# Optimization experiments

Measured on AMD Instinct MI355X. Metric: run time of the kernel, lower is better.

The kernel has to match this reference:

```python
import jax, jax.numpy as jnp
import numpy as np

SEQ, BATCH, IN, HID, OUT = 1024, 2048, 32, 12, 1


def setup_inputs() -> dict:
    key = jax.random.key(0)
    ks = jax.random.split(key, 12)
    s = 0.1
    return {
        "X": jax.random.normal(ks[0], (SEQ, BATCH, IN), dtype=jnp.float32),
        # layer 0 (PyTorch gate order: i, f, g, o)
        "Wih0": jax.random.normal(ks[1], (4 * HID, IN), dtype=jnp.float32) * s,
        "Whh0": jax.random.normal(ks[2], (4 * HID, HID), dtype=jnp.float32) * s,
        "bih0": jax.random.normal(ks[3], (4 * HID,), dtype=jnp.float32) * s,
        "bhh0": jax.random.normal(ks[4], (4 * HID,), dtype=jnp.float32) * s,
        # layer 1
        "Wih1": jax.random.normal(ks[5], (4 * HID, HID), dtype=jnp.float32) * s,
        "Whh1": jax.random.normal(ks[6], (4 * HID, HID), dtype=jnp.float32) * s,
        "bih1": jax.random.normal(ks[7], (4 * HID,), dtype=jnp.float32) * s,
        "bhh1": jax.random.normal(ks[8], (4 * HID,), dtype=jnp.float32) * s,
        # final linear head
        "Wfc": jax.random.normal(ks[9], (OUT, HID), dtype=jnp.float32) * s,
        "bfc": jax.random.normal(ks[10], (OUT,), dtype=jnp.float32) * s,
    }


def _lstm_layer(xs, Wih, Whh, bih, bhh):
    # xs: [S, B, D] seq-first, PyTorch nn.LSTM semantics (gate order i,f,g,o)
    B = xs.shape[1]
    H = Whh.shape[1]
    h0 = jnp.zeros((B, H), xs.dtype)
    c0 = jnp.zeros((B, H), xs.dtype)
    b = bih + bhh

    def step(carry, x_t):
        h, c = carry
        z = x_t @ Wih.T + h @ Whh.T + b  # [B, 4H]
        i, f, g, o = jnp.split(z, 4, axis=-1)
        c = jax.nn.sigmoid(f) * c + jax.nn.sigmoid(i) * jnp.tanh(g)
        h = jax.nn.sigmoid(o) * jnp.tanh(c)
        return (h, c), h

    _, hs = jax.lax.scan(step, (h0, c0), xs)
    return hs  # [S, B, H]


def reference(X, Wih0, Whh0, bih0, bhh0, Wih1, Whh1, bih1, bhh1, Wfc, bfc):
    out = _lstm_layer(X, Wih0, Whh0, bih0, bhh0)
    out = _lstm_layer(out, Wih1, Whh1, bih1, bhh1)
    # faithful to original: out[:, -1, :] on seq-first output selects the
    # LAST BATCH element for every timestep -> [S, H]
    last = out[:, -1, :]
    return last @ Wfc.T + bfc  # [S, OUT]
```

## Files before the change

kernel.cpp:

```cpp
#include <hip/hip_runtime.h>

#define SEQ    1024
#define NBATCH 2048
#define INDIM  32
#define HID    12
#define G4     48
#define NB     (SEQ / 4)
#define NBLK   (NB + 4)
#define CHUNK  16
#define NCH    (SEQ / CHUNK)

#define LOG2E 1.4426950408889634f

typedef float f32x2 __attribute__((ext_vector_type(2)));
typedef float f32x4 __attribute__((ext_vector_type(4)));

template<int CTRL>
__device__ __forceinline__ float qbcast(float v) {
    int x = __builtin_amdgcn_update_dpp(
        0, __builtin_bit_cast(int, v), CTRL, 0xF, 0xF, true);
    return __builtin_bit_cast(float, x);
}
__device__ __forceinline__ float lanebcast(float v, int lane) {
    return __builtin_bit_cast(float,
        __builtin_amdgcn_readlane(__builtin_bit_cast(int, v), lane));
}
__device__ __forceinline__ float sig_part(float zs) {
    return __builtin_amdgcn_rcpf(1.0f + __builtin_amdgcn_exp2f(zs));
}

__global__ __launch_bounds__(256) void lstm_pre(
    const float* __restrict__ X,
    const float* __restrict__ Wih0,
    const float* __restrict__ bih0,
    const float* __restrict__ bhh0,
    float* __restrict__ zx)
{
    int idx = blockIdx.x * blockDim.x + threadIdx.x;
    if (idx >= NBLK * 192) return;
    int b   = idx / 192;
    int rem = idx - b * 192;
    int j   = rem >> 2;
    int q   = rem & 3;
    int t   = 4 * b + q;
    if (t >= SEQ) { zx[idx] = 0.0f; return; }
    int g = j & 3, k = j >> 2;
    int r = g * HID + k;
    const float cexpg = (g == 2) ? (-2.0f * LOG2E) : (-LOG2E);
    const float* x = X + (size_t)t * NBATCH * INDIM + (size_t)(NBATCH - 1) * INDIM;
    const float* w = Wih0 + r * INDIM;
    float za = bih0[r] + bhh0[r], zb = 0.0f;
    #pragma unroll
    for (int kk = 0; kk < INDIM; kk += 2) {
        za = fmaf(w[kk],     x[kk],     za);
        zb = fmaf(w[kk + 1], x[kk + 1], zb);
    }
    zx[idx] = (za + zb) * cexpg;
}

__global__ __launch_bounds__(128) void lstm_seq2(
    const f32x4* __restrict__ zx4,
    float* __restrict__ hbuf,
    const float* __restrict__ Whh0,
    const float* __restrict__ Wih1,
    const float* __restrict__ Whh1,
    const float* __restrict__ bih1,
    const float* __restrict__ bhh1)
{
    __shared__ alignas(16) float lds_h0[(SEQ + 4) * HID];

    const int tid  = threadIdx.x;
    const int wave = tid >> 6;
    const int lane = tid & 63;
    const int jj = (lane < G4) ? lane : 0;
    const int g  = jj & 3;
    const int k  = jj >> 2;
    const int r  = g * HID + k;
    const float cexp = (g == 2) ? (-2.0f * LOG2E) : (-LOG2E);
    const float TSA = -4.0f * LOG2E;
    const float TSB =  2.0f * LOG2E;

    f32x4 wh0[3];
    f32x4 zbE[4], zbO[4];
    f32x4 ph0[3];  float cs0 = 0.0f;
    f32x4 wi1[3], wh1[3];
    f32x4 hb0[4][3], hb1[4][3];
    f32x4 ph1[3];  float cs1 = 0.0f;
    float b1s = 0.0f;

    #pragma unroll
    for (int m = 0; m < 3; ++m) { ph0[m] = f32x4{0,0,0,0}; ph1[m] = f32x4{0,0,0,0}; }

    if (wave == 0) {
        if (lane < G4) lds_h0[SEQ * HID + lane] = 0.0f;
        #pragma unroll
        for (int m = 0; m < 3; ++m)
            wh0[m] = *(const f32x4*)(Whh0 + r * HID + 4 * m) * cexp;
        #pragma unroll
        for (int bb = 0; bb < 4; ++bb) zbE[bb] = zx4[bb * G4 + jj];
    } else {
        #pragma unroll
        for (int m = 0; m < 3; ++m) {
            wi1[m] = *(const f32x4*)(Wih1 + r * HID + 4 * m) * cexp;
            wh1[m] = *(const f32x4*)(Whh1 + r * HID + 4 * m) * cexp;
        }
        b1s = (bih1[r] + bhh1[r]) * cexp;
    }
    __syncthreads();

#define STEPA(zs, t) { \
    f32x4 a0 = __builtin_elementwise_fma(wh0[0], ph0[0], f32x4{(zs), 0.f, 0.f, 0.f}); \
    f32x4 a1 = __builtin_elementwise_fma(wh0[1], ph0[1], f32x4{0.f, 0.f, 0.f, 0.f}); \
    f32x4 a2 = __builtin_elementwise_fma(wh0[2], ph0[2], f32x4{0.f, 0.f, 0.f, 0.f}); \
    f32x4 sv = (a0 + a1) + a2; \
    float z  = (sv.x + sv.y) + (sv.z + sv.w); \
    float rr = sig_part(z); \
    float ai = qbcast<0x00>(rr), af = qbcast<0x55>(rr); \
    float ag = qbcast<0xAA>(rr), ao = qbcast<0xFF>(rr); \
    float igs = ai * fmaf(TSA, ag, TSB); \
    cs0 = fmaf(af, cs0, igs); \
    float rt = sig_part(cs0); \
    float h0 = fmaf(ao + ao, rt, -ao); \
    if (lane < G4 && g == 0) lds_h0[(t) * HID + k] = h0; \
    ph0[0] = f32x4{lanebcast(h0, 0),  lanebcast(h0, 4),  lanebcast(h0, 8),  lanebcast(h0, 12)}; \
    ph0[1] = f32x4{lanebcast(h0, 16), lanebcast(h0, 20), lanebcast(h0, 24), lanebcast(h0, 28)}; \
    ph0[2] = f32x4{lanebcast(h0, 32), lanebcast(h0, 36), lanebcast(h0, 40), lanebcast(h0, 44)}; \
}

#define AITER(cur, nxt, ci) { \
    int cb = 4 * ((ci) + 1); \
    nxt[0] = zx4[(cb + 0) * G4 + jj]; \
    nxt[1] = zx4[(cb + 1) * G4 + jj]; \
    nxt[2] = zx4[(cb + 2) * G4 + jj]; \
    nxt[3] = zx4[(cb + 3) * G4 + jj]; \
    int tA = CHUNK * (ci); \
    STEPA(cur[0].x, tA + 0)  STEPA(cur[0].y, tA + 1)  STEPA(cur[0].z, tA + 2)  STEPA(cur[0].w, tA + 3)  \
    STEPA(cur[1].x, tA + 4)  STEPA(cur[1].y, tA + 5)  STEPA(cur[1].z, tA + 6)  STEPA(cur[1].w, tA + 7)  \
    STEPA(cur[2].x, tA + 8)  STEPA(cur[2].y, tA + 9)  STEPA(cur[2].z, tA + 10) STEPA(cur[2].w, tA + 11) \
    STEPA(cur[3].x, tA + 12) STEPA(cur[3].y, tA + 13) STEPA(cur[3].z, tA + 14) STEPA(cur[3].w, tA + 15) \
}

#define LDGRP(trow, dst) { \
    dst[0][0] = *(const f32x4*)&lds_h0[((trow) + 0) * HID + 0]; \
    dst[0][1] = *(const f32x4*)&lds_h0[((trow) + 0) * HID + 4]; \
    dst[0][2] = *(const f32x4*)&lds_h0[((trow) + 0) * HID + 8]; \
    dst[1][0] = *(const f32x4*)&lds_h0[((trow) + 1) * HID + 0]; \
    dst[1][1] = *(const f32x4*)&lds_h0[((trow) + 1) * HID + 4]; \
    dst[1][2] = *(const f32x4*)&lds_h0[((trow) + 1) * HID + 8]; \
    dst[2][0] = *(const f32x4*)&lds_h0[((trow) + 2) * HID + 0]; \
    dst[2][1] = *(const f32x4*)&lds_h0[((trow) + 2) * HID + 4]; \
    dst[2][2] = *(const f32x4*)&lds_h0[((trow) + 2) * HID + 8]; \
    dst[3][0] = *(const f32x4*)&lds_h0[((trow) + 3) * HID + 0]; \
    dst[3][1] = *(const f32x4*)&lds_h0[((trow) + 3) * HID + 4]; \
    dst[3][2] = *(const f32x4*)&lds_h0[((trow) + 3) * HID + 8]; \
}

#define STEPB(cur, qi, t) { \
    f32x4 a0 = __builtin_elementwise_fma(wi1[0], cur[qi][0], f32x4{b1s, 0.f, 0.f, 0.f}); \
    f32x4 a1 = __builtin_elementwise_fma(wi1[1], cur[qi][1], f32x4{0.f, 0.f, 0.f, 0.f}); \
    f32x4 a2 = __builtin_elementwise_fma(wi1[2], cur[qi][2], f32x4{0.f, 0.f, 0.f, 0.f}); \
    a0 = __builtin_elementwise_fma(wh1[0], ph1[0], a0); \
    a1 = __builtin_elementwise_fma(wh1[1], ph1[1], a1); \
    a2 = __builtin_elementwise_fma(wh1[2], ph1[2], a2); \
    f32x4 sv = (a0 + a1) + a2; \
    float z  = (sv.x + sv.y) + (sv.z + sv.w); \
    float rr = sig_part(z); \
    float ai = qbcast<0x00>(rr), af = qbcast<0x55>(rr); \
    float ag = qbcast<0xAA>(rr), ao = qbcast<0xFF>(rr); \
    float igs = ai * fmaf(TSA, ag, TSB); \
    cs1 = fmaf(af, cs1, igs); \
    float rt = sig_part(cs1); \
    float h1 = fmaf(ao + ao, rt, -ao); \
    if (lane < G4 && g == 0) hbuf[(t) * HID + k] = h1; \
    ph1[0] = f32x4{lanebcast(h1, 0),  lanebcast(h1, 4),  lanebcast(h1, 8),  lanebcast(h1, 12)}; \
    ph1[1] = f32x4{lanebcast(h1, 16), lanebcast(h1, 20), lanebcast(h1, 24), lanebcast(h1, 28)}; \
    ph1[2] = f32x4{lanebcast(h1, 32), lanebcast(h1, 36), lanebcast(h1, 40), lanebcast(h1, 44)}; \
}

#define BGRP(cur, nxt, tload, tproc) { \
    LDGRP((tload), nxt) \
    STEPB(cur, 0, (tproc) + 0) STEPB(cur, 1, (tproc) + 1) \
    STEPB(cur, 2, (tproc) + 2) STEPB(cur, 3, (tproc) + 3) \
}

    for (int i = 0; i < NCH + 2; ++i) {
        if (wave == 0) {
            if (i < NCH) {
                if ((i & 1) == 0) { AITER(zbE, zbO, i) }
                else              { AITER(zbO, zbE, i) }
            }
        } else {
            if (i >= 2) {
                int t0 = (i - 2) * CHUNK;
                if (i == 2) { LDGRP(0, hb0) }
                BGRP(hb0, hb1, t0 + 4,  t0)
                BGRP(hb1, hb0, t0 + 8,  t0 + 4)
                BGRP(hb0, hb1, t0 + 12, t0 + 8)
                BGRP(hb1, hb0, t0 + 16, t0 + 12)
            }
        }
        __syncthreads();
    }
#undef STEPA
#undef AITER
#undef LDGRP
#undef STEPB
#undef BGRP
}

__global__ __launch_bounds__(256) void fc_head(
    const float* __restrict__ hbuf,
    const float* __restrict__ Wfc,
    const float* __restrict__ bfc,
    float* __restrict__ out)
{
    int t = blockIdx.x * blockDim.x + threadIdx.x;
    if (t >= SEQ) return;
    float o = bfc[0];
    const float* h = hbuf + t * HID;
    #pragma unroll
    for (int kk = 0; kk < HID; ++kk) o = fmaf(Wfc[kk], h[kk], o);
    out[t] = o;
}

__global__ __launch_bounds__(64) void lstm_seq_fb(
    const float* __restrict__ X,
    const float* __restrict__ Wih0,
    const float* __restrict__ bih0,
    const float* __restrict__ bhh0,
    const float* __restrict__ Whh0,
    const float* __restrict__ Wih1,
    const float* __restrict__ Whh1,
    const float* __restrict__ bih1,
    const float* __restrict__ bhh1,
    const float* __restrict__ Wfc,
    const float* __restrict__ bfc,
    float* __restrict__ out)
{
    const int j  = threadIdx.x;
    const int jj = (j < G4) ? j : 0;
    const int g  = jj & 3;
    const int k  = jj >> 2;
    const int r  = g * HID + k;
    const float cexp = (g == 2) ? (-2.0f * LOG2E) : (-LOG2E);
    const float TSA = -4.0f * LOG2E;
    const float TSB =  2.0f * LOG2E;

    float whh0[HID], wih1[HID], whh1[HID], wih0[INDIM], wfc[HID];
    #pragma unroll
    for (int kk = 0; kk < HID; ++kk) {
        whh0[kk] = Whh0[r * HID + kk] * cexp;
        wih1[kk] = Wih1[r * HID + kk] * cexp;
        whh1[kk] = Whh1[r * HID + kk] * cexp;
        wfc[kk]  = Wfc[kk];
    }
    #pragma unroll
    for (int kk = 0; kk < INDIM; ++kk) wih0[kk] = Wih0[r * INDIM + kk] * cexp;
    const float b0 = (bih0[r] + bhh0[r]) * cexp;
    const float b1 = (bih1[r] + bhh1[r]) * cexp;
    const float bias_fc = bfc[0];

    float h0v[HID], h1v[HID];
    #pragma unroll
    for (int kk = 0; kk < HID; ++kk) { h0v[kk] = 0.0f; h1v[kk] = 0.0f; }
    float cs0 = 0.0f, cs1 = 0.0f;

    for (int t = 0; t < SEQ; ++t) {
        const float* x = X + (size_t)t * NBATCH * INDIM
                           + (size_t)(NBATCH - 1) * INDIM;
        float z0 = b0;
        #pragma unroll
        for (int kk = 0; kk < INDIM; ++kk) z0 = fmaf(wih0[kk], x[kk], z0);
        #pragma unroll
        for (int kk = 0; kk < HID; ++kk) z0 = fmaf(whh0[kk], h0v[kk], z0);
        float rr = sig_part(z0);
        float ai = qbcast<0x00>(rr), af = qbcast<0x55>(rr);
        float ag = qbcast<0xAA>(rr), ao = qbcast<0xFF>(rr);
        cs0 = fmaf(af, cs0, ai * fmaf(TSA, ag, TSB));
        float rt = sig_part(cs0);
        float h0 = fmaf(ao + ao, rt, -ao);
        #pragma unroll
        for (int kk = 0; kk < HID; ++kk) h0v[kk] = lanebcast(h0, 4 * kk);

        float z1 = b1;
        #pragma unroll
        for (int kk = 0; kk < HID; ++kk) {
            z1 = fmaf(wih1[kk], h0v[kk], z1);
            z1 = fmaf(whh1[kk], h1v[kk], z1);
        }
        rr = sig_part(z1);
        ai = qbcast<0x00>(rr); af = qbcast<0x55>(rr);
        ag = qbcast<0xAA>(rr); ao = qbcast<0xFF>(rr);
        cs1 = fmaf(af, cs1, ai * fmaf(TSA, ag, TSB));
        rt = sig_part(cs1);
        float h1 = fmaf(ao + ao, rt, -ao);
        #pragma unroll
        for (int kk = 0; kk < HID; ++kk) h1v[kk] = lanebcast(h1, 4 * kk);

        float o = bias_fc;
        #pragma unroll
        for (int kk = 0; kk < HID; ++kk) o = fmaf(wfc[kk], h1v[kk], o);
        if (j == 0) out[t] = o;
    }
}

extern "C" void kernel_launch(void* const* d_in, const int* in_sizes, int n_in,
                              void* d_out, int out_size, void* d_ws, size_t ws_size,
                              hipStream_t stream) {
    const float* X    = (const float*)d_in[0];
    const float* Wih0 = (const float*)d_in[1];
    const float* Whh0 = (const float*)d_in[2];
    const float* bih0 = (const float*)d_in[3];
    const float* bhh0 = (const float*)d_in[4];
    const float* Wih1 = (const float*)d_in[5];
    const float* Whh1 = (const float*)d_in[6];
    const float* bih1 = (const float*)d_in[7];
    const float* bhh1 = (const float*)d_in[8];
    const float* Wfc  = (const float*)d_in[9];
    const float* bfc  = (const float*)d_in[10];
    float* out = (float*)d_out;

    const size_t zx_floats = (size_t)NBLK * 192;
    const size_t need = (zx_floats + (size_t)SEQ * HID) * sizeof(float);
    if (ws_size >= need) {
        float* zbuf = (float*)d_ws;
        float* hbuf = zbuf + zx_floats;
        lstm_pre<<<(NBLK * 192 + 255) / 256, 256, 0, stream>>>(
            X, Wih0, bih0, bhh0, zbuf);
        lstm_seq2<<<1, 128, 0, stream>>>(
            (const f32x4*)zbuf, hbuf, Whh0, Wih1, Whh1, bih1, bhh1);
        fc_head<<<(SEQ + 255) / 256, 256, 0, stream>>>(hbuf, Wfc, bfc, out);
    } else {
        lstm_seq_fb<<<1, 64, 0, stream>>>(
            X, Wih0, bih0, bhh0, Whh0,
            Wih1, Whh1, bih1, bhh1, Wfc, bfc, out);
    }
}
```

Baseline: 153.6 us.

## Move layer-1 input projection into layer-0 wave via LDS ring buffer

Wave 0 now computes the layer-1 input projection Wih1·h0 plus bias right after each layer-0 step. It writes the result to a 64-step LDS ring buffer instead of storing raw h0 for the whole sequence. Wave 1 then reads one prefetched scalar per step and only does the recurrent Whh1 dot product, which shortens the layer-1 dependency chain and balances work between the two pipelined waves. The dot products are also rewritten as scalar 12-term FMAs with three accumulators instead of f32x4 vector FMAs. The risk is that wave 0 becomes the longer stage, and that the ring-buffer reuse distance depends on the two-chunk lag between waves.

```diff
diff --git a/kernel.cpp b/kernel.cpp
--- a/kernel.cpp
+++ b/kernel.cpp
@@ -12,7 +12,6 @@
 
 #define LOG2E 1.4426950408889634f
 
-typedef float f32x2 __attribute__((ext_vector_type(2)));
 typedef float f32x4 __attribute__((ext_vector_type(4)));
 
 template<int CTRL>
@@ -27,6 +26,15 @@
 }
 __device__ __forceinline__ float sig_part(float zs) {
     return __builtin_amdgcn_rcpf(1.0f + __builtin_amdgcn_exp2f(zs));
+}
+
+#define DOT12(acc_init, W, H, OUT) { \
+    float da = (acc_init), db = 0.f, dc = 0.f; \
+    da = fmaf(H[0], W[0], da); db = fmaf(H[1],  W[1],  db); dc = fmaf(H[2],  W[2],  dc); \
+    da = fmaf(H[3], W[3], da); db = fmaf(H[4],  W[4],  db); dc = fmaf(H[5],  W[5],  dc); \
+    da = fmaf(H[6], W[6], da); db = fmaf(H[7],  W[7],  db); dc = fmaf(H[8],  W[8],  dc); \
+    da = fmaf(H[9], W[9], da); db = fmaf(H[10], W[10], db); dc = fmaf(H[11], W[11], dc); \
+    OUT = (da + db) + dc; \
 }
 
 __global__ __launch_bounds__(256) void lstm_pre(
@@ -58,7 +66,7 @@
     zx[idx] = (za + zb) * cexpg;
 }
 
-__global__ __launch_bounds__(128) void lstm_seq2(
+__global__ __launch_bounds__(128) void lstm_seq3(
     const f32x4* __restrict__ zx4,
     float* __restrict__ hbuf,
     const float* __restrict__ Whh0,
@@ -67,10 +75,10 @@
     const float* __restrict__ bih1,
     const float* __restrict__ bhh1)
 {
-    __shared__ alignas(16) float lds_h0[(SEQ + 4) * HID];
+    __shared__ float ylds[64 * 64];
 
     const int tid  = threadIdx.x;
-    const int wave = tid >> 6;
+    const int wavei = tid >> 6;
     const int lane = tid & 63;
     const int jj = (lane < G4) ? lane : 0;
     const int g  = jj & 3;
@@ -80,51 +88,47 @@
     const float TSA = -4.0f * LOG2E;
     const float TSB =  2.0f * LOG2E;
 
-    f32x4 wh0[3];
+    float wh0a[HID], wi1a[HID];
+    float h0s[HID];  float cs0 = 0.f;
     f32x4 zbE[4], zbO[4];
-    f32x4 ph0[3];  float cs0 = 0.0f;
-    f32x4 wi1[3], wh1[3];
-    f32x4 hb0[4][3], hb1[4][3];
-    f32x4 ph1[3];  float cs1 = 0.0f;
-    float b1s = 0.0f;
-
-    #pragma unroll
-    for (int m = 0; m < 3; ++m) { ph0[m] = f32x4{0,0,0,0}; ph1[m] = f32x4{0,0,0,0}; }
-
-    if (wave == 0) {
-        if (lane < G4) lds_h0[SEQ * HID + lane] = 0.0f;
-        #pragma unroll
-        for (int m = 0; m < 3; ++m)
-            wh0[m] = *(const f32x4*)(Whh0 + r * HID + 4 * m) * cexp;
+    float b1s = 0.f;
+    float wh1b[HID];
+    float h1s[HID];  float cs1 = 0.f;
+    float yv0 = 0.f, yv1 = 0.f, yv2 = 0.f, yv3 = 0.f;
+
+    if (wavei == 0) {
+        #pragma unroll
+        for (int kk = 0; kk < HID; ++kk) {
+            wh0a[kk] = Whh0[r * HID + kk] * cexp;
+            wi1a[kk] = Wih1[r * HID + kk] * cexp;
+            h0s[kk] = 0.f;
+        }
+        b1s = (bih1[r] + bhh1[r]) * cexp;
         #pragma unroll
         for (int bb = 0; bb < 4; ++bb) zbE[bb] = zx4[bb * G4 + jj];
     } else {
         #pragma unroll
-        for (int m = 0; m < 3; ++m) {
-            wi1[m] = *(const f32x4*)(Wih1 + r * HID + 4 * m) * cexp;
-            wh1[m] = *(const f32x4*)(Whh1 + r * HID + 4 * m) * cexp;
+        for (int kk = 0; kk < HID; ++kk) {
+            wh1b[kk] = Whh1[r * HID + kk] * cexp;
+            h1s[kk] = 0.f;
         }
-        b1s = (bih1[r] + bhh1[r]) * cexp;
     }
     __syncthreads();
 
 #define STEPA(zs, t) { \
-    f32x4 a0 = __builtin_elementwise_fma(wh0[0], ph0[0], f32x4{(zs), 0.f, 0.f, 0.f}); \
-    f32x4 a1 = __builtin_elementwise_fma(wh0[1], ph0[1], f32x4{0.f, 0.f, 0.f, 0.f}); \
-    f32x4 a2 = __builtin_elementwise_fma(wh0[2], ph0[2], f32x4{0.f, 0.f, 0.f, 0.f}); \
-    f32x4 sv = (a0 + a1) + a2; \
-    float z  = (sv.x + sv.y) + (sv.z + sv.w); \
-    float rr = sig_part(z); \
+    float z0v; DOT12((zs), wh0a, h0s, z0v) \
+    float rr = sig_part(z0v); \
     float ai = qbcast<0x00>(rr), af = qbcast<0x55>(rr); \
     float ag = qbcast<0xAA>(rr), ao = qbcast<0xFF>(rr); \
-    float igs = ai * fmaf(TSA, ag, TSB); \
-    cs0 = fmaf(af, cs0, igs); \
+    cs0 = fmaf(af, cs0, ai * fmaf(TSA, ag, TSB)); \
     float rt = sig_part(cs0); \
     float h0 = fmaf(ao + ao, rt, -ao); \
-    if (lane < G4 && g == 0) lds_h0[(t) * HID + k] = h0; \
-    ph0[0] = f32x4{lanebcast(h0, 0),  lanebcast(h0, 4),  lanebcast(h0, 8),  lanebcast(h0, 12)}; \
-    ph0[1] = f32x4{lanebcast(h0, 16), lanebcast(h0, 20), lanebcast(h0, 24), lanebcast(h0, 28)}; \
-    ph0[2] = f32x4{lanebcast(h0, 32), lanebcast(h0, 36), lanebcast(h0, 40), lanebcast(h0, 44)}; \
+    h0s[0] = lanebcast(h0, 0);  h0s[1] = lanebcast(h0, 4);  h0s[2]  = lanebcast(h0, 8); \
+    h0s[3] = lanebcast(h0, 12); h0s[4] = lanebcast(h0, 16); h0s[5]  = lanebcast(h0, 20); \
+    h0s[6] = lanebcast(h0, 24); h0s[7] = lanebcast(h0, 28); h0s[8]  = lanebcast(h0, 32); \
+    h0s[9] = lanebcast(h0, 36); h0s[10] = lanebcast(h0, 40); h0s[11] = lanebcast(h0, 44); \
+    float yo; DOT12(b1s, wi1a, h0s, yo) \
+    ylds[(((t) & 63) << 6) + lane] = yo; \
 }
 
 #define AITER(cur, nxt, ci) { \
@@ -140,51 +144,31 @@
     STEPA(cur[3].x, tA + 12) STEPA(cur[3].y, tA + 13) STEPA(cur[3].z, tA + 14) STEPA(cur[3].w, tA + 15) \
 }
 
-#define LDGRP(trow, dst) { \
-    dst[0][0] = *(const f32x4*)&lds_h0[((trow) + 0) * HID + 0]; \
-    dst[0][1] = *(const f32x4*)&lds_h0[((trow) + 0) * HID + 4]; \
-    dst[0][2] = *(const f32x4*)&lds_h0[((trow) + 0) * HID + 8]; \
-    dst[1][0] = *(const f32x4*)&lds_h0[((trow) + 1) * HID + 0]; \
-    dst[1][1] = *(const f32x4*)&lds_h0[((trow) + 1) * HID + 4]; \
-    dst[1][2] = *(const f32x4*)&lds_h0[((trow) + 1) * HID + 8]; \
-    dst[2][0] = *(const f32x4*)&lds_h0[((trow) + 2) * HID + 0]; \
-    dst[2][1] = *(const f32x4*)&lds_h0[((trow) + 2) * HID + 4]; \
-    dst[2][2] = *(const f32x4*)&lds_h0[((trow) + 2) * HID + 8]; \
-    dst[3][0] = *(const f32x4*)&lds_h0[((trow) + 3) * HID + 0]; \
-    dst[3][1] = *(const f32x4*)&lds_h0[((trow) + 3) * HID + 4]; \
-    dst[3][2] = *(const f32x4*)&lds_h0[((trow) + 3) * HID + 8]; \
-}
-
-#define STEPB(cur, qi, t) { \
-    f32x4 a0 = __builtin_elementwise_fma(wi1[0], cur[qi][0], f32x4{b1s, 0.f, 0.f, 0.f}); \
-    f32x4 a1 = __builtin_elementwise_fma(wi1[1], cur[qi][1], f32x4{0.f, 0.f, 0.f, 0.f}); \
-    f32x4 a2 = __builtin_elementwise_fma(wi1[2], cur[qi][2], f32x4{0.f, 0.f, 0.f, 0.f}); \
-    a0 = __builtin_elementwise_fma(wh1[0], ph1[0], a0); \
-    a1 = __builtin_elementwise_fma(wh1[1], ph1[1], a1); \
-    a2 = __builtin_elementwise_fma(wh1[2], ph1[2], a2); \
-    f32x4 sv = (a0 + a1) + a2; \
-    float z  = (sv.x + sv.y) + (sv.z + sv.w); \
-    float rr = sig_part(z); \
+#define STEPB(yin, t) { \
+    float z1v; DOT12((yin), wh1b, h1s, z1v) \
+    float rr = sig_part(z1v); \
     float ai = qbcast<0x00>(rr), af = qbcast<0x55>(rr); \
     float ag = qbcast<0xAA>(rr), ao = qbcast<0xFF>(rr); \
-    float igs = ai * fmaf(TSA, ag, TSB); \
-    cs1 = fmaf(af, cs1, igs); \
+    cs1 = fmaf(af, cs1, ai * fmaf(TSA, ag, TSB)); \
     float rt = sig_part(cs1); \
     float h1 = fmaf(ao + ao, rt, -ao); \
     if (lane < G4 && g == 0) hbuf[(t) * HID + k] = h1; \
-    ph1[0] = f32x4{lanebcast(h1, 0),  lanebcast(h1, 4),  lanebcast(h1, 8),  lanebcast(h1, 12)}; \
-    ph1[1] = f32x4{lanebcast(h1, 16), lanebcast(h1, 20), lanebcast(h1, 24), lanebcast(h1, 28)}; \
-    ph1[2] = f32x4{lanebcast(h1, 32), lanebcast(h1, 36), lanebcast(h1, 40), lanebcast(h1, 44)}; \
-}
-
-#define BGRP(cur, nxt, tload, tproc) { \
-    LDGRP((tload), nxt) \
-    STEPB(cur, 0, (tproc) + 0) STEPB(cur, 1, (tproc) + 1) \
-    STEPB(cur, 2, (tproc) + 2) STEPB(cur, 3, (tproc) + 3) \
+    h1s[0] = lanebcast(h1, 0);  h1s[1] = lanebcast(h1, 4);  h1s[2]  = lanebcast(h1, 8); \
+    h1s[3] = lanebcast(h1, 12); h1s[4] = lanebcast(h1, 16); h1s[5]  = lanebcast(h1, 20); \
+    h1s[6] = lanebcast(h1, 24); h1s[7] = lanebcast(h1, 28); h1s[8]  = lanebcast(h1, 32); \
+    h1s[9] = lanebcast(h1, 36); h1s[10] = lanebcast(h1, 40); h1s[11] = lanebcast(h1, 44); \
+}
+
+#define BGRP(t0) { \
+    int rb = ((((t0) + 4) & 63) << 6) + jj; \
+    float n0 = ylds[rb], n1 = ylds[rb + 64], n2 = ylds[rb + 128], n3 = ylds[rb + 192]; \
+    STEPB(yv0, (t0))     STEPB(yv1, (t0) + 1) \
+    STEPB(yv2, (t0) + 2) STEPB(yv3, (t0) + 3) \
+    yv0 = n0; yv1 = n1; yv2 = n2; yv3 = n3; \
 }
 
     for (int i = 0; i < NCH + 2; ++i) {
-        if (wave == 0) {
+        if (wavei == 0) {
             if (i < NCH) {
                 if ((i & 1) == 0) { AITER(zbE, zbO, i) }
                 else              { AITER(zbO, zbE, i) }
@@ -192,18 +176,17 @@
         } else {
             if (i >= 2) {
                 int t0 = (i - 2) * CHUNK;
-                if (i == 2) { LDGRP(0, hb0) }
-                BGRP(hb0, hb1, t0 + 4,  t0)
-                BGRP(hb1, hb0, t0 + 8,  t0 + 4)
-                BGRP(hb0, hb1, t0 + 12, t0 + 8)
-                BGRP(hb1, hb0, t0 + 16, t0 + 12)
+                if (i == 2) {
+                    yv0 = ylds[jj];       yv1 = ylds[64 + jj];
+                    yv2 = ylds[128 + jj]; yv3 = ylds[192 + jj];
+                }
+                BGRP(t0) BGRP(t0 + 4) BGRP(t0 + 8) BGRP(t0 + 12)
             }
         }
         __syncthreads();
     }
 #undef STEPA
 #undef AITER
-#undef LDGRP
 #undef STEPB
 #undef BGRP
 }
@@ -327,7 +310,7 @@
         float* hbuf = zbuf + zx_floats;
         lstm_pre<<<(NBLK * 192 + 255) / 256, 256, 0, stream>>>(
             X, Wih0, bih0, bhh0, zbuf);
-        lstm_seq2<<<1, 128, 0, stream>>>(
+        lstm_seq3<<<1, 128, 0, stream>>>(
             (const f32x4*)zbuf, hbuf, Whh0, Wih1, Whh1, bih1, bhh1);
         fc_head<<<(SEQ + 255) / 256, 256, 0, stream>>>(hbuf, Wfc, bfc, out);
     } else {
```

Result: faster. 135.8 us (-11.6%).
